# Kernel optimization log

Measured on AMD Instinct MI355X. Metric: run time of the kernel, lower is better.

## Reference

```python
import jax, jax.numpy as jnp
import numpy as np
import math

N_HEADS = 16
D_Q = 1024
D_K = 1024
D_V = 1024
D_OUT = 1024
HID = D_OUT // N_HEADS  # 64
BATCH = 2
SEQ = 2048


def setup_inputs() -> dict:
    key = jax.random.key(0)
    ks = jax.random.split(key, 7)
    stdv = 1.0 / math.sqrt(HID)
    so = 1.0 / math.sqrt(D_OUT)
    return {
        "q": jax.random.normal(ks[0], (BATCH, SEQ, D_Q), dtype=jnp.float32),
        "k": jax.random.normal(ks[1], (BATCH, SEQ, D_K), dtype=jnp.float32),
        "v": jax.random.normal(ks[2], (BATCH, SEQ, D_V), dtype=jnp.float32),
        "W_query": jax.random.uniform(ks[3], (N_HEADS, D_Q, HID), jnp.float32, -stdv, stdv),
        "W_key": jax.random.uniform(ks[4], (N_HEADS, D_K, HID), jnp.float32, -stdv, stdv),
        "W_val": jax.random.uniform(ks[5], (N_HEADS, D_V, HID), jnp.float32, -stdv, stdv),
        "W_out": jax.random.uniform(ks[6], (N_HEADS, HID, D_OUT), jnp.float32, -so, so),
    }


def reference(q, k, v, W_query, W_key, W_val, W_out):
    norm = 1.0 / math.sqrt(HID)
    # per-head projections: [h, b, s, e]
    Q = jnp.einsum("bqd,hde->hbqe", q, W_query)
    K = jnp.einsum("bkd,hde->hbke", k, W_key)
    V = jnp.einsum("bkd,hde->hbke", v, W_val)
    # scaled dot-product attention
    compat = norm * jnp.einsum("hbqe,hbke->hbqk", Q, K)
    attn = jax.nn.softmax(compat, axis=-1)
    heads = jnp.einsum("hbqk,hbke->hbqe", attn, V)
    # output projection: concat heads then W_out == sum over h of per-head proj
    out = jnp.einsum("hbqe,heo->bqo", heads, W_out)
    return out
```

## Files before the change

kernel.cpp:

```cpp
#include <hip/hip_runtime.h>
#include <hip/hip_bf16.h>

typedef __bf16 bf16;
typedef __bf16 bf16x8 __attribute__((ext_vector_type(8)));
typedef __bf16 bf16x4 __attribute__((ext_vector_type(4)));
typedef float  f32x4  __attribute__((ext_vector_type(4)));

#define MFMA16(a,b,c) __builtin_amdgcn_mfma_f32_16x16x32_bf16(a, b, c, 0, 0, 0)

__device__ __forceinline__ void gl2lds16(const bf16* g, bf16* l) {
    __builtin_amdgcn_global_load_lds(
        (__attribute__((address_space(1))) void*)g,
        (__attribute__((address_space(3))) void*)l, 16, 0, 0);
}

__global__ __launch_bounds__(256)
void prep_kernel(const float* __restrict__ q, const float* __restrict__ k,
                 const float* __restrict__ v, const float* __restrict__ Wq,
                 const float* __restrict__ Wk, const float* __restrict__ Wv,
                 const float* __restrict__ Wo, bf16* __restrict__ Xcat,
                 bf16* __restrict__ Wqkv, bf16* __restrict__ Wot)
{
    __shared__ bf16 Tl[64][72];
    const int bid = blockIdx.x;
    const int tid = threadIdx.x;

    if (bid < 6144) {
        int gidx = bid * 256 + tid;
        int t    = gidx >> 19;
        int off  = (gidx & 0x7FFFF) * 8;
        const float* src = (t == 0) ? q : (t == 1) ? k : v;
        const float4 f0 = *(const float4*)&src[off];
        const float4 f1 = *(const float4*)&src[off + 4];
        bf16x8 p = { (bf16)f0.x, (bf16)f0.y, (bf16)f0.z, (bf16)f0.w,
                     (bf16)f1.x, (bf16)f1.y, (bf16)f1.z, (bf16)f1.w };
        *(bf16x8*)&Xcat[(size_t)gidx * 8] = p;
        return;
    }
    if (bid < 6912) {
        int idx = bid - 6144;
        int x = idx & 15, z = idx >> 4;
        int t = z >> 4, h = z & 15;
        const float* inp = ((t == 0) ? Wq : (t == 1) ? Wk : Wv) + (size_t)h * 65536;
        bf16* outp = Wqkv + (size_t)t * 1024 * 1024 + (size_t)h * 65536;
        int r0 = x * 64;
        #pragma unroll
        for (int i = 0; i < 2; i++) {
            int s = tid + i * 256;
            int r = s >> 3, c8 = (s & 7) * 8;
            const float* ap = &inp[(size_t)(r0 + r) * 64 + c8];
            float4 f0 = *(const float4*)ap;
            float4 f1 = *(const float4*)(ap + 4);
            bf16x8 p = { (bf16)f0.x, (bf16)f0.y, (bf16)f0.z, (bf16)f0.w,
                         (bf16)f1.x, (bf16)f1.y, (bf16)f1.z, (bf16)f1.w };
            *(bf16x8*)&Tl[r][c8] = p;
        }
        __syncthreads();
        #pragma unroll
        for (int i = 0; i < 2; i++) {
            int s = tid + i * 256;
            int c = s >> 3, r8 = (s & 7) * 8;
            bf16x8 p;
            #pragma unroll
            for (int j = 0; j < 8; j++) p[j] = Tl[r8 + j][c];
            *(bf16x8*)&outp[(size_t)c * 1024 + r0 + r8] = p;
        }
        return;
    }
    {
        int idx = bid - 6912;
        int y = idx & 15, h = idx >> 4;
        int c0 = y * 64;
        const float* inp = Wo + (size_t)h * 65536;
        bf16* outp = Wot + (size_t)h * 64;
        #pragma unroll
        for (int i = 0; i < 2; i++) {
            int s = tid + i * 256;
            int r = s >> 3, c8 = (s & 7) * 8;
            const float* ap = &inp[(size_t)r * 1024 + c0 + c8];
            float4 f0 = *(const float4*)ap;
            float4 f1 = *(const float4*)(ap + 4);
            bf16x8 p = { (bf16)f0.x, (bf16)f0.y, (bf16)f0.z, (bf16)f0.w,
                         (bf16)f1.x, (bf16)f1.y, (bf16)f1.z, (bf16)f1.w };
            *(bf16x8*)&Tl[r][c8] = p;
        }
        __syncthreads();
        #pragma unroll
        for (int i = 0; i < 2; i++) {
            int s = tid + i * 256;
            int c = s >> 3, r8 = (s & 7) * 8;
            bf16x8 p;
            #pragma unroll
            for (int j = 0; j < 8; j++) p[j] = Tl[r8 + j][c];
            *(bf16x8*)&outp[(size_t)(c0 + c) * 1024 + r8] = p;
        }
    }
}

__global__ __launch_bounds__(256)
void qkv_gemm(const bf16* __restrict__ Xcat, const bf16* __restrict__ Wqkv,
              bf16* __restrict__ Cq, bf16* __restrict__ Ck, bf16* __restrict__ Vt,
              float qscale)
{
    __shared__ bf16 Al[2][128 * 32];
    __shared__ bf16 Bl[2][128 * 32];
    const int slab  = blockIdx.x >> 5;
    const int mbase = (blockIdx.x & 31) * 128;
    const int nbase = blockIdx.y * 128;
    const int tid = threadIdx.x;
    const int w = tid >> 6, lane = tid & 63;
    const int lm = lane & 15, q4 = lane >> 4;
    const int wr = (w >> 1) * 64, wc = (w & 1) * 64;
    const int lrow = lane >> 2;
    const int lsw  = ((lane & 3) ^ ((lane >> 3) & 3)) * 8;

    const bf16* A  = Xcat + (size_t)slab * 4096 * 1024;
    const bf16* Bt = Wqkv + (size_t)slab * 1024 * 1024;

    f32x4 acc[4][4] = {};

    auto stage = [&](int k0, int d) {
        #pragma unroll
        for (int i = 0; i < 2; i++) {
            int c = w * 2 + i;
            gl2lds16(&A [(size_t)(mbase + c * 16 + lrow) * 1024 + k0 + lsw], &Al[d][c * 512]);
            gl2lds16(&Bt[(size_t)(nbase + c * 16 + lrow) * 1024 + k0 + lsw], &Bl[d][c * 512]);
        }
    };

    stage(0, 0);

    for (int t = 0; t < 32; t++) {
        __syncthreads();
        if (t < 31) stage((t + 1) * 32, (t + 1) & 1);
        const bf16* Ad = &Al[t & 1][0];
        const bf16* Bd = &Bl[t & 1][0];
        __builtin_amdgcn_s_setprio(1);
        {
            bf16x8 a[4], bfr[4];
            const int g = (q4 ^ ((lm >> 1) & 3)) * 8;
            #pragma unroll
            for (int i = 0; i < 4; i++) a[i]   = *(const bf16x8*)&Ad[(wr + i * 16 + lm) * 32 + g];
            #pragma unroll
            for (int j = 0; j < 4; j++) bfr[j] = *(const bf16x8*)&Bd[(wc + j * 16 + lm) * 32 + g];
            #pragma unroll
            for (int i = 0; i < 4; i++)
                #pragma unroll
                for (int j = 0; j < 4; j++)
                    acc[i][j] = MFMA16(a[i], bfr[j], acc[i][j]);
        }
        __builtin_amdgcn_s_setprio(0);
    }

    if (slab == 2) {
        #pragma unroll
        for (int i = 0; i < 4; i++)
            #pragma unroll
            for (int j = 0; j < 4; j++) {
                int s0  = mbase + wr + i * 16 + q4 * 4;
                int col = nbase + wc + j * 16 + lm;
                int sp  = (s0 & ~31) | (((s0 >> 2) & 3) * 8) | (((s0 >> 4) & 1) * 4);
                bf16x4 p = { (bf16)acc[i][j][0], (bf16)acc[i][j][1],
                             (bf16)acc[i][j][2], (bf16)acc[i][j][3] };
                *(bf16x4*)&Vt[(size_t)col * 4096 + sp] = p;
            }
    } else {
        bf16* C = (slab == 0) ? Cq : Ck;
        const float scale = (slab == 0) ? qscale : 1.0f;
        #pragma unroll
        for (int i = 0; i < 4; i++)
            #pragma unroll
            for (int j = 0; j < 4; j++)
                #pragma unroll
                for (int r = 0; r < 4; r++) {
                    int row = mbase + wr + i * 16 + q4 * 4 + r;
                    int col = nbase + wc + j * 16 + lm;
                    C[(size_t)row * 1024 + col] = (bf16)(acc[i][j][r] * scale);
                }
    }
}

__global__ __launch_bounds__(256)
void outproj_gemm(const bf16* __restrict__ A, const bf16* __restrict__ Bt,
                  float* __restrict__ C)
{
    __shared__ bf16 Al[2][64 * 64];
    __shared__ bf16 Bl[2][128 * 64];
    const int mbase = blockIdx.x * 64;
    const int nbase = blockIdx.y * 128;
    const int tid = threadIdx.x;
    const int w = tid >> 6, lane = tid & 63;
    const int lm = lane & 15, q4 = lane >> 4;
    const int wm = (w >> 1) * 32, wn = (w & 1) * 64;
    const int lrow = lane >> 3, lsw = ((lane & 7) ^ lrow) * 8;

    f32x4 acc[2][4] = {};

    auto stage = [&](int k0, int d) {
        #pragma unroll
        for (int i = 0; i < 2; i++) {
            int c = w * 2 + i;
            gl2lds16(&A[(size_t)(mbase + c * 8 + lrow) * 1024 + k0 + lsw], &Al[d][c * 512]);
        }
        #pragma unroll
        for (int i = 0; i < 4; i++) {
            int c = w * 4 + i;
            gl2lds16(&Bt[(size_t)(nbase + c * 8 + lrow) * 1024 + k0 + lsw], &Bl[d][c * 512]);
        }
    };

    stage(0, 0);

    for (int t = 0; t < 16; t++) {
        __syncthreads();
        if (t < 15) stage((t + 1) * 64, (t + 1) & 1);
        const bf16* Ad = &Al[t & 1][0];
        const bf16* Bd = &Bl[t & 1][0];
        __builtin_amdgcn_s_setprio(1);
        #pragma unroll
        for (int kk2 = 0; kk2 < 2; kk2++) {
            bf16x8 a[2], bfr[4];
            const int g = ((kk2 * 4 + q4) ^ (lm & 7)) * 8;
            #pragma unroll
            for (int i = 0; i < 2; i++) a[i]   = *(const bf16x8*)&Ad[(wm + i * 16 + lm) * 64 + g];
            #pragma unroll
            for (int j = 0; j < 4; j++) bfr[j] = *(const bf16x8*)&Bd[(wn + j * 16 + lm) * 64 + g];
            #pragma unroll
            for (int i = 0; i < 2; i++)
                #pragma unroll
                for (int j = 0; j < 4; j++)
                    acc[i][j] = MFMA16(a[i], bfr[j], acc[i][j]);
        }
        __builtin_amdgcn_s_setprio(0);
    }

    #pragma unroll
    for (int i = 0; i < 2; i++)
        #pragma unroll
        for (int j = 0; j < 4; j++)
            #pragma unroll
            for (int r = 0; r < 4; r++) {
                int row = mbase + wm + i * 16 + q4 * 4 + r;
                int col = nbase + wn + j * 16 + lm;
                C[(size_t)row * 1024 + col] = acc[i][j][r];
            }
}

__global__ __launch_bounds__(256, 2)
void attn_kernel(const bf16* __restrict__ Qp, const bf16* __restrict__ Kp,
                 const bf16* __restrict__ Vt, bf16* __restrict__ Hd)
{
    __shared__ bf16 Kl[2][2][64 * 64];
    __shared__ bf16 Vl[2][2][64 * 64];
    __shared__ float Ls[128];

    const int n  = blockIdx.x + 16 * (blockIdx.y + 2 * blockIdx.z);
    const int m  = (n & 7) * 64 + (n >> 3);
    const int qt = m & 15, bh = m >> 4;
    const int b  = bh & 1,  h  = bh >> 1;

    const int qbase = qt * 128;
    const int tid  = threadIdx.x;
    const int w    = tid >> 6, lane = tid & 63;
    const int p    = w & 1;
    const int kvh  = w >> 1;
    const int lm   = lane & 15, q4 = lane >> 4;
    const int lrow = lane >> 3, lsw = ((lane & 7) ^ lrow) * 8;

    const bf16* Qh = Qp + (size_t)(b * 2048 + qbase + p * 64) * 1024 + h * 64;
    const bf16* Kh = Kp + (size_t)(b * 2048) * 1024 + h * 64;
    const bf16* Vh = Vt + (size_t)(h * 64) * 4096 + b * 2048;

    bf16x8 Qf[4][2];
    #pragma unroll
    for (int i = 0; i < 4; i++)
        #pragma unroll
        for (int kk2 = 0; kk2 < 2; kk2++)
            Qf[i][kk2] = *(const bf16x8*)&Qh[(size_t)(i * 16 + lm) * 1024 + kk2 * 32 + q4 * 8];

    const bf16 one = (bf16)1.0f;
    const bf16x8 ones = { one, one, one, one, one, one, one, one };

    f32x4 O[4][4] = {};
    f32x4 Lacc[4] = {};

    auto stage = [&](int kt, int d) {
        #pragma unroll
        for (int i = 0; i < 4; i++) {
            int c = w * 4 + i;
            gl2lds16(&Kh[(size_t)(kt * 128 + c * 8 + lrow) * 1024 + lsw],
                     &Kl[d][c >> 3][(c & 7) * 512]);
            gl2lds16(&Vh[(size_t)((c & 7) * 8 + lrow) * 4096 + kt * 128 + (c >> 3) * 64 + lsw],
                     &Vl[d][c >> 3][(c & 7) * 512]);
        }
    };

    auto Sc = [&](const bf16* Kd, f32x4 (&St)[4][2]) {
        #pragma unroll
        for (int c2 = 0; c2 < 2; c2++) {
            const int ctp = kvh * 2 + c2;
            #pragma unroll
            for (int kk2 = 0; kk2 < 2; kk2++) {
                const int g = ((kk2 * 4 + q4) ^ (lm & 7)) * 8;
                bf16x8 kf = *(const bf16x8*)&Kd[(ctp * 16 + lm) * 64 + g];
                #pragma unroll
                for (int i = 0; i < 4; i++)
                    St[i][c2] = MFMA16(kf, Qf[i][kk2], St[i][c2]);
            }
        }
    };

    auto PVc = [&](const bf16* Vd, const f32x4 (&St)[4][2]) {
        bf16x8 Pf[4];
        #pragma unroll
        for (int i = 0; i < 4; i++)
            #pragma unroll
            for (int j = 0; j < 8; j++)
                Pf[i][j] = (bf16)__builtin_amdgcn_exp2f(St[i][j >> 2][j & 3]);
        __builtin_amdgcn_s_setprio(1);
        #pragma unroll
        for (int i = 0; i < 4; i++) Lacc[i] = MFMA16(Pf[i], ones, Lacc[i]);
        const int gv = ((kvh * 4 + q4) ^ (lm & 7)) * 8;
        #pragma unroll
        for (int et = 0; et < 4; et++) {
            bf16x8 vf = *(const bf16x8*)&Vd[(et * 16 + lm) * 64 + gv];
            #pragma unroll
            for (int i = 0; i < 4; i++)
                O[i][et] = MFMA16(Pf[i], vf, O[i][et]);
        }
        __builtin_amdgcn_s_setprio(0);
    };

    stage(0, 0);

    for (int it = 0; it < 16; it++) {
        __syncthreads();
        if (it < 15) stage(it + 1, (it + 1) & 1);
        const int d = it & 1;

        f32x4 St0[4][2] = {}, St1[4][2] = {};
        __builtin_amdgcn_s_setprio(1);
        Sc(&Kl[d][0][0], St0);
        Sc(&Kl[d][1][0], St1);
        __builtin_amdgcn_s_setprio(0);
        PVc(&Vl[d][0][0], St0);
        PVc(&Vl[d][1][0], St1);
    }

    __syncthreads();
    float* Ol = (float*)&Kl[0][0][0];
    if (kvh == 1) {
        #pragma unroll
        for (int i = 0; i < 4; i++)
            #pragma unroll
            for (int et = 0; et < 4; et++)
                #pragma unroll
                for (int r = 0; r < 4; r++)
                    Ol[(p * 64 + i * 16 + q4 * 4 + r) * 64 + et * 16 + lm] = O[i][et][r];
        if (lm == 0) {
            #pragma unroll
            for (int i = 0; i < 4; i++)
                #pragma unroll
                for (int r = 0; r < 4; r++)
                    Ls[p * 64 + i * 16 + q4 * 4 + r] = Lacc[i][r];
        }
    }
    __syncthreads();
    if (kvh == 0) {
        #pragma unroll
        for (int i = 0; i < 4; i++) {
            float rl[4];
            #pragma unroll
            for (int r = 0; r < 4; r++)
                rl[r] = 1.0f / (Lacc[i][r] + Ls[p * 64 + i * 16 + q4 * 4 + r]);
            #pragma unroll
            for (int et = 0; et < 4; et++)
                #pragma unroll
                for (int r = 0; r < 4; r++) {
                    float o = O[i][et][r] +
                              Ol[(p * 64 + i * 16 + q4 * 4 + r) * 64 + et * 16 + lm];
                    int row = b * 2048 + qbase + p * 64 + i * 16 + q4 * 4 + r;
                    Hd[(size_t)row * 1024 + h * 64 + et * 16 + lm] = (bf16)(o * rl[r]);
                }
        }
    }
}

extern "C" void kernel_launch(void* const* d_in, const int* in_sizes, int n_in,
                              void* d_out, int out_size, void* d_ws, size_t ws_size,
                              hipStream_t stream)
{
    const float* q  = (const float*)d_in[0];
    const float* k  = (const float*)d_in[1];
    const float* v  = (const float*)d_in[2];
    const float* Wq = (const float*)d_in[3];
    const float* Wk = (const float*)d_in[4];
    const float* Wv = (const float*)d_in[5];
    const float* Wo = (const float*)d_in[6];
    float* out = (float*)d_out;

    const size_t Mi = 1024 * 1024;
    bf16* Xcat  = (bf16*)d_ws;
    bf16* Hd    = Xcat;
    bf16* Wqkv  = Xcat + 12 * Mi;
    bf16* Wot   = Xcat + 15 * Mi;
    bf16* Qproj = Xcat + 16 * Mi;
    bf16* Kproj = Xcat + 20 * Mi;
    bf16* Vtb   = (bf16*)d_out;

    const float qscale = 0.125f * 1.4426950408889634f;

    prep_kernel<<<7168, 256, 0, stream>>>(q, k, v, Wq, Wk, Wv, Wo, Xcat, Wqkv, Wot);
    qkv_gemm<<<dim3(96, 8), 256, 0, stream>>>(Xcat, Wqkv, Qproj, Kproj, Vtb, qscale);
    attn_kernel<<<dim3(16, 2, 16), 256, 0, stream>>>(Qproj, Kproj, Vtb, Hd);
    outproj_gemm<<<dim3(64, 8), 256, 0, stream>>>(Hd, Wot, out);
}
```

Before: 198.1 us.

## Fuse fp32-to-bf16 activation conversion into QKV GEMM A-tile loading

The prep kernel no longer converts the q/k/v activations to a bf16 workspace. The QKV GEMM now reads fp32 activations directly into registers, converts them, and writes them to LDS after the MFMA block, overlapping the loads with compute. This removes a full write and re-read of the 24 MB bf16 copy. In exchange each GEMM block reads twice as many bytes per A tile and now converts on every N-tile, since each A row is read by 8 column blocks. Separately, the s_setprio hints are removed from the attention kernel.

```diff
diff --git a/kernel.cpp b/kernel.cpp
--- a/kernel.cpp
+++ b/kernel.cpp
@@ -15,30 +15,16 @@
 }
 
 __global__ __launch_bounds__(256)
-void prep_kernel(const float* __restrict__ q, const float* __restrict__ k,
-                 const float* __restrict__ v, const float* __restrict__ Wq,
-                 const float* __restrict__ Wk, const float* __restrict__ Wv,
-                 const float* __restrict__ Wo, bf16* __restrict__ Xcat,
+void prep_kernel(const float* __restrict__ Wq, const float* __restrict__ Wk,
+                 const float* __restrict__ Wv, const float* __restrict__ Wo,
                  bf16* __restrict__ Wqkv, bf16* __restrict__ Wot)
 {
     __shared__ bf16 Tl[64][72];
     const int bid = blockIdx.x;
     const int tid = threadIdx.x;
 
-    if (bid < 6144) {
-        int gidx = bid * 256 + tid;
-        int t    = gidx >> 19;
-        int off  = (gidx & 0x7FFFF) * 8;
-        const float* src = (t == 0) ? q : (t == 1) ? k : v;
-        const float4 f0 = *(const float4*)&src[off];
-        const float4 f1 = *(const float4*)&src[off + 4];
-        bf16x8 p = { (bf16)f0.x, (bf16)f0.y, (bf16)f0.z, (bf16)f0.w,
-                     (bf16)f1.x, (bf16)f1.y, (bf16)f1.z, (bf16)f1.w };
-        *(bf16x8*)&Xcat[(size_t)gidx * 8] = p;
-        return;
-    }
-    if (bid < 6912) {
-        int idx = bid - 6144;
+    if (bid < 768) {
+        int idx = bid;
         int x = idx & 15, z = idx >> 4;
         int t = z >> 4, h = z & 15;
         const float* inp = ((t == 0) ? Wq : (t == 1) ? Wk : Wv) + (size_t)h * 65536;
@@ -68,7 +54,7 @@
         return;
     }
     {
-        int idx = bid - 6912;
+        int idx = bid - 768;
         int y = idx & 15, h = idx >> 4;
         int c0 = y * 64;
         const float* inp = Wo + (size_t)h * 65536;
@@ -98,7 +84,8 @@
 }
 
 __global__ __launch_bounds__(256)
-void qkv_gemm(const bf16* __restrict__ Xcat, const bf16* __restrict__ Wqkv,
+void qkv_gemm(const float* __restrict__ q, const float* __restrict__ k,
+              const float* __restrict__ v, const bf16* __restrict__ Wqkv,
               bf16* __restrict__ Cq, bf16* __restrict__ Ck, bf16* __restrict__ Vt,
               float qscale)
 {
@@ -114,25 +101,48 @@
     const int lrow = lane >> 2;
     const int lsw  = ((lane & 3) ^ ((lane >> 3) & 3)) * 8;
 
-    const bf16* A  = Xcat + (size_t)slab * 4096 * 1024;
+    const float* A = (slab == 0) ? q : (slab == 1) ? k : v;
     const bf16* Bt = Wqkv + (size_t)slab * 1024 * 1024;
 
     f32x4 acc[4][4] = {};
-
-    auto stage = [&](int k0, int d) {
+    float4 Ar[2][2];
+
+    auto loadA = [&](int k0) {
         #pragma unroll
         for (int i = 0; i < 2; i++) {
             int c = w * 2 + i;
-            gl2lds16(&A [(size_t)(mbase + c * 16 + lrow) * 1024 + k0 + lsw], &Al[d][c * 512]);
+            const float* ap = &A[(size_t)(mbase + c * 16 + lrow) * 1024 + k0 + lsw];
+            Ar[i][0] = *(const float4*)ap;
+            Ar[i][1] = *(const float4*)(ap + 4);
+        }
+    };
+    auto writeA = [&](int d) {
+        #pragma unroll
+        for (int i = 0; i < 2; i++) {
+            int c = w * 2 + i;
+            bf16x8 pk = { (bf16)Ar[i][0].x, (bf16)Ar[i][0].y,
+                          (bf16)Ar[i][0].z, (bf16)Ar[i][0].w,
+                          (bf16)Ar[i][1].x, (bf16)Ar[i][1].y,
+                          (bf16)Ar[i][1].z, (bf16)Ar[i][1].w };
+            *(bf16x8*)&Al[d][c * 512 + lane * 8] = pk;
+        }
+    };
+    auto stageB = [&](int k0, int d) {
+        #pragma unroll
+        for (int i = 0; i < 2; i++) {
+            int c = w * 2 + i;
             gl2lds16(&Bt[(size_t)(nbase + c * 16 + lrow) * 1024 + k0 + lsw], &Bl[d][c * 512]);
         }
     };
 
-    stage(0, 0);
+    loadA(0); writeA(0); stageB(0, 0);
 
     for (int t = 0; t < 32; t++) {
         __syncthreads();
-        if (t < 31) stage((t + 1) * 32, (t + 1) & 1);
+        if (t < 31) {
+            loadA((t + 1) * 32);
+            stageB((t + 1) * 32, (t + 1) & 1);
+        }
         const bf16* Ad = &Al[t & 1][0];
         const bf16* Bd = &Bl[t & 1][0];
         __builtin_amdgcn_s_setprio(1);
@@ -150,6 +160,7 @@
                     acc[i][j] = MFMA16(a[i], bfr[j], acc[i][j]);
         }
         __builtin_amdgcn_s_setprio(0);
+        if (t < 31) writeA((t + 1) & 1);
     }
 
     if (slab == 2) {
@@ -317,7 +328,6 @@
             #pragma unroll
             for (int j = 0; j < 8; j++)
                 Pf[i][j] = (bf16)__builtin_amdgcn_exp2f(St[i][j >> 2][j & 3]);
-        __builtin_amdgcn_s_setprio(1);
         #pragma unroll
         for (int i = 0; i < 4; i++) Lacc[i] = MFMA16(Pf[i], ones, Lacc[i]);
         const int gv = ((kvh * 4 + q4) ^ (lm & 7)) * 8;
@@ -328,7 +338,6 @@
             for (int i = 0; i < 4; i++)
                 O[i][et] = MFMA16(Pf[i], vf, O[i][et]);
         }
-        __builtin_amdgcn_s_setprio(0);
     };
 
     stage(0, 0);
@@ -339,10 +348,8 @@
         const int d = it & 1;
 
         f32x4 St0[4][2] = {}, St1[4][2] = {};
-        __builtin_amdgcn_s_setprio(1);
         Sc(&Kl[d][0][0], St0);
         Sc(&Kl[d][1][0], St1);
-        __builtin_amdgcn_s_setprio(0);
         PVc(&Vl[d][0][0], St0);
         PVc(&Vl[d][1][0], St1);
     }
@@ -400,18 +407,17 @@
     float* out = (float*)d_out;
 
     const size_t Mi = 1024 * 1024;
-    bf16* Xcat  = (bf16*)d_ws;
-    bf16* Hd    = Xcat;
-    bf16* Wqkv  = Xcat + 12 * Mi;
-    bf16* Wot   = Xcat + 15 * Mi;
-    bf16* Qproj = Xcat + 16 * Mi;
-    bf16* Kproj = Xcat + 20 * Mi;
+    bf16* Hd    = (bf16*)d_ws;
+    bf16* Wqkv  = (bf16*)d_ws + 12 * Mi;
+    bf16* Wot   = (bf16*)d_ws + 15 * Mi;
+    bf16* Qproj = (bf16*)d_ws + 16 * Mi;
+    bf16* Kproj = (bf16*)d_ws + 20 * Mi;
     bf16* Vtb   = (bf16*)d_out;
 
     const float qscale = 0.125f * 1.4426950408889634f;
 
-    prep_kernel<<<7168, 256, 0, stream>>>(q, k, v, Wq, Wk, Wv, Wo, Xcat, Wqkv, Wot);
-    qkv_gemm<<<dim3(96, 8), 256, 0, stream>>>(Xcat, Wqkv, Qproj, Kproj, Vtb, qscale);
+    prep_kernel<<<1024, 256, 0, stream>>>(Wq, Wk, Wv, Wo, Wqkv, Wot);
+    qkv_gemm<<<dim3(96, 8), 256, 0, stream>>>(q, k, v, Wqkv, Qproj, Kproj, Vtb, qscale);
     attn_kernel<<<dim3(16, 2, 16), 256, 0, stream>>>(Qproj, Kproj, Vtb, Hd);
     outproj_gemm<<<dim3(64, 8), 256, 0, stream>>>(Hd, Wot, out);
 }
```

Result: slower. 205.0 us (+3.5%).
